# Kernel optimization log

Hardware: AMD Instinct MI355X
Metric: run time of the kernel (lower is better)

Reference implementation:

```python
import jax, jax.numpy as jnp
import numpy as np

N, L, C = 4, 1024, 512   # batch, frames, channels (in_channels == mdl_channels)
H = 16                   # heads
D = C // H               # head dim
S = 16                   # number of segments for bi
EPS_PN = 1e-5            # MaskPowerNorm / GroupScaling eps


def setup_inputs() -> dict:
    key = jax.random.key(0)
    ks = jax.random.split(key, 8)
    x = jax.random.normal(ks[0], (N, L, C), jnp.float32)
    bi = jnp.sort(jax.random.randint(ks[1], (L,), 0, S)).astype(jnp.int64)
    w_qkv = jax.random.normal(ks[2], (3 * C, C), jnp.float32) * 0.02
    w_beta = jax.random.normal(ks[3], (1, 3 * C), jnp.float32) * 0.02
    w1 = jax.random.normal(ks[4], (C, C), jnp.float32) * 0.02
    b1 = jnp.zeros((C,), jnp.float32)
    w2 = jax.random.normal(ks[5], (C, C), jnp.float32) * 0.02
    b2 = jnp.zeros((C,), jnp.float32)
    pn1_w = jnp.ones((C,), jnp.float32)
    pn1_b = jnp.zeros((C,), jnp.float32)
    pn1_phi = jnp.ones((C,), jnp.float32)
    pn2_w = jnp.ones((C,), jnp.float32)
    pn2_b = jnp.zeros((C,), jnp.float32)
    pn2_phi = jnp.ones((C,), jnp.float32)
    return dict(x=x, bi=bi, w_qkv=w_qkv, w_beta=w_beta, w1=w1, b1=b1, w2=w2,
                b2=b2, pn1_w=pn1_w, pn1_b=pn1_b, pn1_phi=pn1_phi,
                pn2_w=pn2_w, pn2_b=pn2_b, pn2_phi=pn2_phi)


def power_norm(x, weight, bias, running_phi):
    # MaskPowerNorm (eval): GroupScaling1D over H channel groups, then
    # x / sqrt(running_phi + eps) * weight + bias
    n, l, c = x.shape
    cg = c // H
    g = x.reshape(n, l, H, cg)
    m2 = jnp.mean(g * g, axis=-1, keepdims=True)
    gs = (g / jnp.sqrt(m2 + EPS_PN)).reshape(n, l, c)
    return gs / jnp.sqrt(running_phi + EPS_PN) * weight + bias


def reference(x, bi, w_qkv, w_beta, w1, b1, w2, b2,
              pn1_w, pn1_b, pn1_phi, pn2_w, pn2_b, pn2_phi):
    n, l, c = x.shape
    d = c // H
    # QKV projection (bias=False)
    qkv = x @ w_qkv.T                                  # (n, l, 3c)
    q, k, v = jnp.split(qkv, 3, axis=-1)
    q = q.reshape(n, l, H, d)
    k = k.reshape(n, l, H, d)
    v = v.reshape(n, l, H, d)
    # elu feature map on temperature-scaled q, k
    temp = d ** (-0.25)
    phi = lambda t: jax.nn.elu(t * temp) + 1.0
    q = phi(q).transpose(0, 2, 1, 3)                   # (n, h, l, d)
    k = phi(k).transpose(0, 2, 1, 3)                   # (n, h, l, d)
    vt = v.transpose(0, 2, 1, 3)                       # (n, h, l, d)
    # per-position outer products k v^T : (n, h, l, d, d)
    kv = k[..., :, None] * vt[..., None, :]
    # scatter_sum over frames into S segments, then gather back per frame
    kv_seg = jnp.zeros((n, H, S, d, d), kv.dtype).at[:, :, bi].add(kv)
    kv_g = kv_seg[:, :, bi]                            # (n, h, l, d, d)
    k_seg = jnp.zeros((n, H, S, d), k.dtype).at[:, :, bi].add(k)
    k_g = k_seg[:, :, bi]                              # (n, h, l, d)
    z = 1.0 / jnp.sum(q * k_g, axis=-1)                # (n, h, l)
    v_out = jnp.einsum('nhld,nhldm->nhlm', q, kv_g) * z[..., None]
    t = v_out.transpose(0, 2, 1, 3).reshape(n, l, c)   # (n, l, c)
    # AddNorm with beta gate (dropout is identity in eval)
    beta = jax.nn.sigmoid(jnp.concatenate([t, x, t - x], axis=-1) @ w_beta.T)
    x1 = power_norm(beta * x + (1.0 - beta) * t, pn1_w, pn1_b, pn1_phi)
    # FFN (exact GELU) + AddNorm (no beta)
    ff = jax.nn.gelu(x1 @ w1.T + b1, approximate=False) @ w2.T + b2
    return power_norm(ff + x1, pn2_w, pn2_b, pn2_phi)
```

## Files before the change

### kernel.cpp

```cpp
#include <hip/hip_runtime.h>
#include <math.h>

#define NB 4
#define LB 1024
#define CB 512
#define HH 16
#define DD 32
#define SS 16
#define NL (NB*LB)
#define C3 (3*CB)

typedef __attribute__((ext_vector_type(8))) short short8;
typedef __attribute__((ext_vector_type(4))) float f32x4;

#define GL16(gp, lp) __builtin_amdgcn_global_load_lds( \
    (const __attribute__((address_space(1))) void*)(gp), \
    (__attribute__((address_space(3))) void*)(lp), 16, 0, 0)

__device__ __forceinline__ unsigned short f2bf_rn(float f) {
  unsigned u = __builtin_bit_cast(unsigned, f);
  unsigned r = u + 0x7FFFu + ((u >> 16) & 1u);
  return (unsigned short)(r >> 16);
}
__device__ __forceinline__ float bf2f(unsigned short h) {
  unsigned u = ((unsigned)h) << 16;
  return __builtin_bit_cast(float, u);
}

__device__ __forceinline__ int lower_bound_i32(const int* a, int n, int v) {
  int lo = 0, hi = n;
  while (lo < hi) { int mid = (lo + hi) >> 1; if (a[mid] < v) lo = mid + 1; else hi = mid; }
  return lo;
}

#define X4T   524288
#define WQ4T  720896
#define W14T  786432
#define TOT4  851968
__global__ __launch_bounds__(256) void split_conv(
    const float* __restrict__ x, const float* __restrict__ wqkv,
    const float* __restrict__ w1, const float* __restrict__ w2,
    ushort* __restrict__ xh, ushort* __restrict__ xl,
    ushort* __restrict__ wqh, ushort* __restrict__ wql,
    ushort* __restrict__ w1h, ushort* __restrict__ w1l,
    ushort* __restrict__ w2h, ushort* __restrict__ w2l)
{
  for (int idx = blockIdx.x * 256 + threadIdx.x; idx < TOT4; idx += gridDim.x * 256) {
    const float* src; ushort *dh, *dl; int off;
    if (idx < X4T)        { src = x;    dh = xh;  dl = xl;  off = idx; }
    else if (idx < WQ4T)  { src = wqkv; dh = wqh; dl = wql; off = idx - X4T; }
    else if (idx < W14T)  { src = w1;   dh = w1h; dl = w1l; off = idx - WQ4T; }
    else                  { src = w2;   dh = w2h; dl = w2l; off = idx - W14T; }
    const float4 v = ((const float4*)src)[off];
    ushort4 h, l;
    h.x = f2bf_rn(v.x); l.x = f2bf_rn(v.x - bf2f(h.x));
    h.y = f2bf_rn(v.y); l.y = f2bf_rn(v.y - bf2f(h.y));
    h.z = f2bf_rn(v.z); l.z = f2bf_rn(v.z - bf2f(h.z));
    h.w = f2bf_rn(v.w); l.w = f2bf_rn(v.w - bf2f(h.w));
    ((ushort4*)dh)[off] = h;
    ((ushort4*)dl)[off] = l;
  }
}

template<int MODE, int BN>
__global__ __launch_bounds__(256) void gemm_mfma2(
    const ushort* __restrict__ Ah, const ushort* __restrict__ Al,
    const ushort* __restrict__ Bh, const ushort* __restrict__ Bl,
    int M, int Nn, int K,
    const float* __restrict__ bias,
    float* __restrict__ Cf, ushort* __restrict__ Ch, ushort* __restrict__ Cl,
    const ushort* __restrict__ resh, const ushort* __restrict__ resl)
{
  constexpr int NJ = BN / 32;
  __shared__ short8 AhL[512], AlL[512];
  __shared__ short8 BhL[4*BN], BlL[4*BN];
  const int tid = threadIdx.x;
  const int w = tid >> 6, l = tid & 63;
  const int wm = w >> 1, wn = w & 1;
  const int l15 = l & 15, l4 = l >> 4;
  const int bm = blockIdx.x * 128, bn = blockIdx.y * BN;

  f32x4 acc[4][NJ];
  #pragma unroll
  for (int i = 0; i < 4; ++i)
    #pragma unroll
    for (int j = 0; j < NJ; ++j)
      acc[i][j] = {0.f, 0.f, 0.f, 0.f};

  for (int k0 = 0; k0 < K; k0 += 32) {
    if (k0) __syncthreads();
    #pragma unroll
    for (int i = 0; i < 2; ++i) {
      const int pb = i * 256 + w * 64;
      const int p  = pb + l;
      const long go = (long)(bm + (p & 127)) * K + k0 + (p >> 7) * 8;
      GL16(Ah + go, (char*)AhL + pb * 16);
      GL16(Al + go, (char*)AlL + pb * 16);
    }
    if (BN == 128) {
      #pragma unroll
      for (int i = 0; i < 2; ++i) {
        const int pb = i * 256 + w * 64;
        const int p  = pb + l;
        const long go = (long)(bn + (p & 127)) * K + k0 + (p >> 7) * 8;
        GL16(Bh + go, (char*)BhL + pb * 16);
        GL16(Bl + go, (char*)BlL + pb * 16);
      }
    } else {
      const int pb = w * 64;
      const int p  = pb + l;
      const long go = (long)(bn + (p & 63)) * K + k0 + (p >> 6) * 8;
      GL16(Bh + go, (char*)BhL + pb * 16);
      GL16(Bl + go, (char*)BlL + pb * 16);
    }
    __syncthreads();

    short8 bhf[NJ], blf[NJ];
    #pragma unroll
    for (int j = 0; j < NJ; ++j) {
      const int idx = l4 * BN + wn * (NJ * 16) + j * 16 + l15;
      bhf[j] = BhL[idx]; blf[j] = BlL[idx];
    }
    #pragma unroll
    for (int i = 0; i < 4; ++i) {
      const int idx = l4 * 128 + wm * 64 + i * 16 + l15;
      const short8 ah = AhL[idx], al = AlL[idx];
      #pragma unroll
      for (int j = 0; j < NJ; ++j) {
        acc[i][j] = __builtin_amdgcn_mfma_f32_16x16x32_bf16(ah, bhf[j], acc[i][j], 0, 0, 0);
        acc[i][j] = __builtin_amdgcn_mfma_f32_16x16x32_bf16(ah, blf[j], acc[i][j], 0, 0, 0);
        acc[i][j] = __builtin_amdgcn_mfma_f32_16x16x32_bf16(al, bhf[j], acc[i][j], 0, 0, 0);
      }
    }
  }

  const float temp = 0.42044820762685725f;
  #pragma unroll
  for (int i = 0; i < 4; ++i) {
    #pragma unroll
    for (int j = 0; j < NJ; ++j) {
      const int n  = bn + wn * (NJ * 16) + j * 16 + l15;
      const int mb = bm + wm * 64 + i * 16 + l4 * 4;
      #pragma unroll
      for (int r = 0; r < 4; ++r) {
        const int m = mb + r;
        float v = acc[i][j][r];
        if (MODE == 0) {
          if (n < 2 * CB) { const float z = v * temp; v = (z > 0.f) ? (z + 1.f) : expf(z); }
          Cf[(long)m * Nn + n] = v;
        } else if (MODE == 1) {
          v += bias[n];
          v = v * 0.5f * (1.f + erff(v * 0.70710678118654752f));
          const ushort hb = f2bf_rn(v);
          Ch[(long)m * Nn + n] = hb;
          Cl[(long)m * Nn + n] = f2bf_rn(v - bf2f(hb));
        } else {
          const long o = (long)m * Nn + n;
          v += bias[n] + bf2f(resh[o]) + bf2f(resl[o]);
          Cf[o] = v;
        }
      }
    }
  }
}

__global__ __launch_bounds__(256) void seg_attn(
    const float* __restrict__ qkv, const int* __restrict__ bi,
    float* __restrict__ tbuf)
{
  const int b = blockIdx.x;
  const int s = b & (SS-1);
  const int h = (b >> 4) & (HH-1);
  const int n = b >> 8;
  __shared__ float ks[32][DD];
  __shared__ float vs[32][DD];
  __shared__ float KVs[DD][DD];
  __shared__ float Ks[DD];
  __shared__ int sb[2];
  const int tid = threadIdx.x;
  if (tid == 0) {
    sb[0] = lower_bound_i32(bi, LB, s);
    sb[1] = lower_bound_i32(bi, LB, s + 1);
  }
  __syncthreads();
  const int lo = sb[0], hi = sb[1];
  const int srow = tid >> 3, sq = tid & 7;
  const int d = tid >> 3, m0 = (tid & 7) * 4;
  float4 acc = make_float4(0.f, 0.f, 0.f, 0.f);
  float ksum = 0.f;

  for (int l0 = lo; l0 < hi; l0 += 32) {
    const int lr = l0 + srow;
    if (lr < hi) {
      const float* row = qkv + (long)(n*LB + lr) * C3 + h*DD;
      *(float4*)&ks[srow][sq*4] = *(const float4*)(row + CB   + sq*4);
      *(float4*)&vs[srow][sq*4] = *(const float4*)(row + 2*CB + sq*4);
    } else {
      *(float4*)&ks[srow][sq*4] = make_float4(0.f,0.f,0.f,0.f);
      *(float4*)&vs[srow][sq*4] = make_float4(0.f,0.f,0.f,0.f);
    }
    __syncthreads();
    #pragma unroll
    for (int r = 0; r < 32; ++r) {
      const float kd = ks[r][d];
      ksum += kd;
      const float4 vv = *(const float4*)&vs[r][m0];
      acc.x = fmaf(kd, vv.x, acc.x);
      acc.y = fmaf(kd, vv.y, acc.y);
      acc.z = fmaf(kd, vv.z, acc.z);
      acc.w = fmaf(kd, vv.w, acc.w);
    }
    __syncthreads();
  }
  *(float4*)&KVs[d][m0] = acc;
  if ((tid & 7) == 0) Ks[d] = ksum;
  __syncthreads();

  const int prow = tid >> 5, m = tid & 31;
  for (int l0 = lo; l0 < hi; l0 += 32) {
    const int lr = l0 + srow;
    if (lr < hi)
      *(float4*)&ks[srow][sq*4] = *(const float4*)(qkv + (long)(n*LB + lr) * C3 + h*DD + sq*4);
    __syncthreads();
    #pragma unroll
    for (int step = 0; step < 4; ++step) {
      const int r  = step * 8 + prow;
      const int l2 = l0 + r;
      if (l2 < hi) {
        float vo = 0.f, den = 0.f;
        #pragma unroll
        for (int d2 = 0; d2 < DD; ++d2) {
          const float qd = ks[r][d2];
          vo  = fmaf(qd, KVs[d2][m], vo);
          den = fmaf(qd, Ks[d2], den);
        }
        tbuf[(long)(n*LB + l2) * CB + h*DD + m] = vo / den;
      }
    }
    __syncthreads();
  }
}

__global__ __launch_bounds__(256) void beta_pn1(
    const float* __restrict__ x, const float* __restrict__ tbuf,
    const float* __restrict__ w_beta,
    const float* __restrict__ pw, const float* __restrict__ pb, const float* __restrict__ pphi,
    ushort* __restrict__ x1h, ushort* __restrict__ x1l)
{
  const int row = blockIdx.x;
  const int tid = threadIdx.x;
  const int c0 = tid * 2;
  const long base = (long)row * CB;
  const float2 xv = *(const float2*)&x[base + c0];
  const float2 tv = *(const float2*)&tbuf[base + c0];
  float p = tv.x * w_beta[c0]   + xv.x * w_beta[CB + c0]   + (tv.x - xv.x) * w_beta[2*CB + c0]
          + tv.y * w_beta[c0+1] + xv.y * w_beta[CB + c0+1] + (tv.y - xv.y) * w_beta[2*CB + c0+1];
  #pragma unroll
  for (int off = 32; off >= 1; off >>= 1) p += __shfl_xor(p, off, 64);
  __shared__ float red[4];
  if ((tid & 63) == 0) red[tid >> 6] = p;
  __syncthreads();
  const float zsum = red[0] + red[1] + red[2] + red[3];
  const float beta = 1.f / (1.f + expf(-zsum));
  const float y0 = beta * xv.x + (1.f - beta) * tv.x;
  const float y1 = beta * xv.y + (1.f - beta) * tv.y;
  float ss = y0*y0 + y1*y1;
  #pragma unroll
  for (int off = 1; off < 16; off <<= 1) ss += __shfl_xor(ss, off, 64);
  const float inv = rsqrtf(ss * (1.f/32.f) + 1e-5f);
  const float o0 = y0 * inv * rsqrtf(pphi[c0]   + 1e-5f) * pw[c0]   + pb[c0];
  const float o1 = y1 * inv * rsqrtf(pphi[c0+1] + 1e-5f) * pw[c0+1] + pb[c0+1];
  const ushort h0 = f2bf_rn(o0), h1 = f2bf_rn(o1);
  const ushort g0 = f2bf_rn(o0 - bf2f(h0)), g1 = f2bf_rn(o1 - bf2f(h1));
  *(ushort2*)&x1h[base + c0] = make_ushort2(h0, h1);
  *(ushort2*)&x1l[base + c0] = make_ushort2(g0, g1);
}

__global__ __launch_bounds__(256) void pn2_kernel(
    const float* __restrict__ ffx,
    const float* __restrict__ pw, const float* __restrict__ pb, const float* __restrict__ pphi,
    float* __restrict__ out)
{
  const int row = blockIdx.x;
  const int tid = threadIdx.x;
  const int c0 = tid * 2;
  const long base = (long)row * CB;
  const float2 yv = *(const float2*)&ffx[base + c0];
  float ss = yv.x*yv.x + yv.y*yv.y;
  #pragma unroll
  for (int off = 1; off < 16; off <<= 1) ss += __shfl_xor(ss, off, 64);
  const float inv = rsqrtf(ss * (1.f/32.f) + 1e-5f);
  const float o0 = yv.x * inv * rsqrtf(pphi[c0]   + 1e-5f) * pw[c0]   + pb[c0];
  const float o1 = yv.y * inv * rsqrtf(pphi[c0+1] + 1e-5f) * pw[c0+1] + pb[c0+1];
  *(float2*)&out[base + c0] = make_float2(o0, o1);
}

extern "C" void kernel_launch(void* const* d_in, const int* in_sizes, int n_in,
                              void* d_out, int out_size, void* d_ws, size_t ws_size,
                              hipStream_t stream)
{
  const float* x       = (const float*)d_in[0];
  const int*   bi      = (const int*)d_in[1];
  const float* w_qkv   = (const float*)d_in[2];
  const float* w_beta  = (const float*)d_in[3];
  const float* w1      = (const float*)d_in[4];
  const float* b1      = (const float*)d_in[5];
  const float* w2      = (const float*)d_in[6];
  const float* b2      = (const float*)d_in[7];
  const float* pn1_w   = (const float*)d_in[8];
  const float* pn1_b   = (const float*)d_in[9];
  const float* pn1_phi = (const float*)d_in[10];
  const float* pn2_w   = (const float*)d_in[11];
  const float* pn2_b   = (const float*)d_in[12];
  const float* pn2_phi = (const float*)d_in[13];
  float* out = (float*)d_out;
  char*  wsb = (char*)d_ws;

  ushort* wqh  = (ushort*)(wsb);
  ushort* wql  = (ushort*)(wsb +  1572864);
  ushort* w1h  = (ushort*)(wsb +  3145728);
  ushort* w1l  = (ushort*)(wsb +  3670016);
  ushort* w2h  = (ushort*)(wsb +  4194304);
  ushort* w2l  = (ushort*)(wsb +  4718592);
  ushort* xh   = (ushort*)(wsb +  5242880);
  ushort* xl   = (ushort*)(wsb +  9437184);
  float*  tbuf = (float*) (wsb +  5242880);
  float*  qkvb = (float*) (wsb + 13631488);
  ushort* x1h  = (ushort*)(wsb + 13631488);
  ushort* x1l  = (ushort*)(wsb + 17825792);
  ushort* h1h  = (ushort*)(wsb + 22020096);
  ushort* h1l  = (ushort*)(wsb + 26214400);
  float*  ffx  = (float*) (wsb + 30408704);

  split_conv<<<2048, 256, 0, stream>>>(x, w_qkv, w1, w2,
                                       xh, xl, wqh, wql, w1h, w1l, w2h, w2l);
  gemm_mfma2<0,128><<<dim3(NL/128, C3/128), 256, 0, stream>>>(
      xh, xl, wqh, wql, NL, C3, CB, nullptr, qkvb, nullptr, nullptr, nullptr, nullptr);
  seg_attn<<<NB*HH*SS, 256, 0, stream>>>(qkvb, bi, tbuf);
  beta_pn1<<<NL, 256, 0, stream>>>(x, tbuf, w_beta, pn1_w, pn1_b, pn1_phi, x1h, x1l);
  gemm_mfma2<1,64><<<dim3(NL/128, CB/64), 256, 0, stream>>>(
      x1h, x1l, w1h, w1l, NL, CB, CB, b1, nullptr, h1h, h1l, nullptr, nullptr);
  gemm_mfma2<2,64><<<dim3(NL/128, CB/64), 256, 0, stream>>>(
      h1h, h1l, w2h, w2l, NL, CB, CB, b2, ffx, nullptr, nullptr, x1h, x1l);
  pn2_kernel<<<NL, 256, 0, stream>>>(ffx, pn2_w, pn2_b, pn2_phi, out);
}
```

Baseline: 223.4 us.

## Double-buffer GEMM LDS tiles and shrink FFN GEMM M-tile to 64

Rewrites the split-bf16 MFMA GEMM so the LDS tiles are double-buffered. The next K-slice is loaded by global_load_lds while the current slice feeds the MFMAs, which leaves one barrier per iteration. The FFN GEMMs also move to 64x64 tiles, doubling their grid size for better occupancy of the CUs. The cost is twice the LDS per block and less reuse per tile in the FFN GEMMs.

```diff
diff --git a/kernel.cpp b/kernel.cpp
--- a/kernel.cpp
+++ b/kernel.cpp
@@ -62,8 +62,8 @@
   }
 }
 
-template<int MODE, int BN>
-__global__ __launch_bounds__(256) void gemm_mfma2(
+template<int MODE, int BM, int BN>
+__global__ __launch_bounds__(256) void gemm_mfma3(
     const ushort* __restrict__ Ah, const ushort* __restrict__ Al,
     const ushort* __restrict__ Bh, const ushort* __restrict__ Bl,
     int M, int Nn, int K,
@@ -71,59 +71,60 @@
     float* __restrict__ Cf, ushort* __restrict__ Ch, ushort* __restrict__ Cl,
     const ushort* __restrict__ resh, const ushort* __restrict__ resl)
 {
+  constexpr int MI = BM / 32;
   constexpr int NJ = BN / 32;
-  __shared__ short8 AhL[512], AlL[512];
-  __shared__ short8 BhL[4*BN], BlL[4*BN];
+  constexpr int ASLOT = BM * 4;
+  constexpr int BSLOT = BN * 4;
+  __shared__ short8 AhL[2*ASLOT], AlL[2*ASLOT];
+  __shared__ short8 BhL[2*BSLOT], BlL[2*BSLOT];
   const int tid = threadIdx.x;
   const int w = tid >> 6, l = tid & 63;
   const int wm = w >> 1, wn = w & 1;
   const int l15 = l & 15, l4 = l >> 4;
-  const int bm = blockIdx.x * 128, bn = blockIdx.y * BN;
-
-  f32x4 acc[4][NJ];
-  #pragma unroll
-  for (int i = 0; i < 4; ++i)
+  const int bm = blockIdx.x * BM, bn = blockIdx.y * BN;
+
+  f32x4 acc[MI][NJ];
+  #pragma unroll
+  for (int i = 0; i < MI; ++i)
     #pragma unroll
     for (int j = 0; j < NJ; ++j)
       acc[i][j] = {0.f, 0.f, 0.f, 0.f};
 
-  for (int k0 = 0; k0 < K; k0 += 32) {
-    if (k0) __syncthreads();
-    #pragma unroll
-    for (int i = 0; i < 2; ++i) {
-      const int pb = i * 256 + w * 64;
-      const int p  = pb + l;
-      const long go = (long)(bm + (p & 127)) * K + k0 + (p >> 7) * 8;
-      GL16(Ah + go, (char*)AhL + pb * 16);
-      GL16(Al + go, (char*)AlL + pb * 16);
-    }
-    if (BN == 128) {
-      #pragma unroll
-      for (int i = 0; i < 2; ++i) {
-        const int pb = i * 256 + w * 64;
-        const int p  = pb + l;
-        const long go = (long)(bn + (p & 127)) * K + k0 + (p >> 7) * 8;
-        GL16(Bh + go, (char*)BhL + pb * 16);
-        GL16(Bl + go, (char*)BlL + pb * 16);
-      }
-    } else {
-      const int pb = w * 64;
-      const int p  = pb + l;
-      const long go = (long)(bn + (p & 63)) * K + k0 + (p >> 6) * 8;
-      GL16(Bh + go, (char*)BhL + pb * 16);
-      GL16(Bl + go, (char*)BlL + pb * 16);
-    }
-    __syncthreads();
-
+  const int NT = K / 32;
+
+  auto stage = [&](int buf, int k0) {
+    #pragma unroll
+    for (int i = 0; i < ASLOT/256; ++i) {
+      const int pb = buf*ASLOT + i*256 + w*64;
+      const int p  = i*256 + w*64 + l;
+      const long go = (long)(bm + (p & (BM-1))) * K + k0 + (p / BM) * 8;
+      GL16(Ah + go, (char*)AhL + pb*16);
+      GL16(Al + go, (char*)AlL + pb*16);
+    }
+    #pragma unroll
+    for (int i = 0; i < BSLOT/256; ++i) {
+      const int pb = buf*BSLOT + i*256 + w*64;
+      const int p  = i*256 + w*64 + l;
+      const long go = (long)(bn + (p & (BN-1))) * K + k0 + (p / BN) * 8;
+      GL16(Bh + go, (char*)BhL + pb*16);
+      GL16(Bl + go, (char*)BlL + pb*16);
+    }
+  };
+
+  stage(0, 0);
+  __syncthreads();
+  int cur = 0;
+  for (int t = 0; t < NT; ++t) {
+    if (t + 1 < NT) stage(cur ^ 1, (t + 1) * 32);
     short8 bhf[NJ], blf[NJ];
     #pragma unroll
     for (int j = 0; j < NJ; ++j) {
-      const int idx = l4 * BN + wn * (NJ * 16) + j * 16 + l15;
+      const int idx = cur*BSLOT + l4*BN + wn*(BN/2) + j*16 + l15;
       bhf[j] = BhL[idx]; blf[j] = BlL[idx];
     }
     #pragma unroll
-    for (int i = 0; i < 4; ++i) {
-      const int idx = l4 * 128 + wm * 64 + i * 16 + l15;
+    for (int i = 0; i < MI; ++i) {
+      const int idx = cur*ASLOT + l4*BM + wm*(BM/2) + i*16 + l15;
       const short8 ah = AhL[idx], al = AlL[idx];
       #pragma unroll
       for (int j = 0; j < NJ; ++j) {
@@ -132,15 +133,17 @@
         acc[i][j] = __builtin_amdgcn_mfma_f32_16x16x32_bf16(al, bhf[j], acc[i][j], 0, 0, 0);
       }
     }
+    __syncthreads();
+    cur ^= 1;
   }
 
   const float temp = 0.42044820762685725f;
   #pragma unroll
-  for (int i = 0; i < 4; ++i) {
+  for (int i = 0; i < MI; ++i) {
     #pragma unroll
     for (int j = 0; j < NJ; ++j) {
-      const int n  = bn + wn * (NJ * 16) + j * 16 + l15;
-      const int mb = bm + wm * 64 + i * 16 + l4 * 4;
+      const int n  = bn + wn * (BN/2) + j * 16 + l15;
+      const int mb = bm + wm * (BM/2) + i * 16 + l4 * 4;
       #pragma unroll
       for (int r = 0; r < 4; ++r) {
         const int m = mb + r;
@@ -334,13 +337,13 @@
 
   split_conv<<<2048, 256, 0, stream>>>(x, w_qkv, w1, w2,
                                        xh, xl, wqh, wql, w1h, w1l, w2h, w2l);
-  gemm_mfma2<0,128><<<dim3(NL/128, C3/128), 256, 0, stream>>>(
+  gemm_mfma3<0,128,128><<<dim3(NL/128, C3/128), 256, 0, stream>>>(
       xh, xl, wqh, wql, NL, C3, CB, nullptr, qkvb, nullptr, nullptr, nullptr, nullptr);
   seg_attn<<<NB*HH*SS, 256, 0, stream>>>(qkvb, bi, tbuf);
   beta_pn1<<<NL, 256, 0, stream>>>(x, tbuf, w_beta, pn1_w, pn1_b, pn1_phi, x1h, x1l);
-  gemm_mfma2<1,64><<<dim3(NL/128, CB/64), 256, 0, stream>>>(
+  gemm_mfma3<1,64,64><<<dim3(NL/64, CB/64), 256, 0, stream>>>(
       x1h, x1l, w1h, w1l, NL, CB, CB, b1, nullptr, h1h, h1l, nullptr, nullptr);
-  gemm_mfma2<2,64><<<dim3(NL/128, CB/64), 256, 0, stream>>>(
+  gemm_mfma3<2,64,64><<<dim3(NL/64, CB/64), 256, 0, stream>>>(
       h1h, h1l, w2h, w2l, NL, CB, CB, b2, ffx, nullptr, nullptr, x1h, x1l);
   pn2_kernel<<<NL, 256, 0, stream>>>(ffx, pn2_w, pn2_b, pn2_phi, out);
 }
```

Result: faster. 204.2 us (-8.6%).
